# Optimization experiments

Measured on AMD Instinct MI355X. Metric: run time of the kernel, lower is better.

## Reference

```python
import jax, jax.numpy as jnp
import numpy as np

DIM = 512
HEADS = 8
HEAD_DIM = DIM // HEADS


def setup_inputs() -> dict:
    key = jax.random.key(0)
    ks = jax.random.split(key, 8)
    B, T, C, H, W = 2, 8, DIM, 16, 16
    s = lambda fan: 1.0 / np.sqrt(fan)
    return {
        "features_seq": jax.random.normal(ks[0], (B, T, C, H, W), jnp.float32),
        # weights stored as [in, out] (math identical to torch Linear y = x @ W.T)
        "qkv_w": jax.random.normal(ks[1], (C, 3 * C), jnp.float32) * s(C),
        "qkv_b": jnp.zeros((3 * C,), jnp.float32),
        "proj_w": jax.random.normal(ks[2], (C, C), jnp.float32) * s(C),
        "proj_b": jnp.zeros((C,), jnp.float32),
        "ln1_g": jnp.ones((C,), jnp.float32),
        "ln1_b": jnp.zeros((C,), jnp.float32),
        "w1": jax.random.normal(ks[3], (C, 4 * C), jnp.float32) * s(C),
        "b1": jnp.zeros((4 * C,), jnp.float32),
        "w2": jax.random.normal(ks[4], (4 * C, C), jnp.float32) * s(4 * C),
        "b2": jnp.zeros((C,), jnp.float32),
        "ln2_g": jnp.ones((C,), jnp.float32),
        "ln2_b": jnp.zeros((C,), jnp.float32),
    }


def _layernorm(x, g, b, eps=1e-5):
    mu = jnp.mean(x, axis=-1, keepdims=True)
    var = jnp.var(x, axis=-1, keepdims=True)
    return (x - mu) * jax.lax.rsqrt(var + eps) * g + b


def _mhsa(x, qkv_w, qkv_b, proj_w, proj_b):
    B, N, C = x.shape
    qkv = (x @ qkv_w + qkv_b).reshape(B, N, 3, HEADS, HEAD_DIM)
    qkv = jnp.transpose(qkv, (2, 0, 3, 1, 4))  # [3, B, h, N, d]
    q, k, v = qkv[0], qkv[1], qkv[2]
    scale = HEAD_DIM ** -0.5
    attn = jnp.einsum("bhqd,bhkd->bhqk", q, k) * scale
    attn = jax.nn.softmax(attn, axis=-1)
    o = jnp.einsum("bhqk,bhkd->bhqd", attn, v)
    o = jnp.transpose(o, (0, 2, 1, 3)).reshape(B, N, C)
    return o @ proj_w + proj_b


def reference(features_seq, qkv_w, qkv_b, proj_w, proj_b, ln1_g, ln1_b,
              w1, b1, w2, b2, ln2_g, ln2_b):
    B, T, C, H, W = features_seq.shape
    L = H * W
    # [B,T,C,H,W] -> [B, T*L, C]
    x = features_seq.reshape(B, T, C, L).transpose(0, 1, 3, 2).reshape(B, T * L, C)
    x = x + _mhsa(_layernorm(x, ln1_g, ln1_b), qkv_w, qkv_b, proj_w, proj_b)
    h = _layernorm(x, ln2_g, ln2_b)
    h = jax.nn.gelu(h @ w1 + b1, approximate=False) @ w2 + b2
    x = x + h
    # back to [B, T, C, H, W]
    out = x.reshape(B, T, L, C).transpose(0, 1, 3, 2).reshape(B, T, C, H, W)
    return out
```

## Files before the change

kernel.cpp:

```cpp
#include <hip/hip_runtime.h>
#include <stdint.h>
#include <math.h>

typedef __attribute__((ext_vector_type(8))) short short8;
typedef __attribute__((ext_vector_type(4))) float f32x4;
typedef __attribute__((ext_vector_type(4))) ushort ushort4v;

__device__ __forceinline__ ushort f2bf(float f) {
    union { float f; uint32_t i; } v; v.f = f;
    uint32_t r = v.i + 0x7FFFu + ((v.i >> 16) & 1u);
    return (ushort)(r >> 16);
}
__device__ __forceinline__ float bf2f(ushort u) {
    union { uint32_t i; float f; } v; v.i = ((uint32_t)u) << 16; return v.f;
}

__device__ __forceinline__ void gload_lds16(const ushort* gp, ushort* lp) {
    __builtin_amdgcn_global_load_lds(
        (const __attribute__((address_space(1))) void*)gp,
        (__attribute__((address_space(3))) void*)lp, 16, 0, 0);
}

__global__ __launch_bounds__(512) void prep_kernel(const float* __restrict__ in,
        const float* __restrict__ g, const float* __restrict__ bta,
        float* __restrict__ x, ushort* __restrict__ xln) {
    int token = blockIdx.x;
    int c = threadIdx.x;
    int b = token >> 11;
    int n = token & 2047;
    int t = n >> 8;
    int l = n & 255;
    size_t iidx = (((size_t)((b * 8 + t) * 512 + c)) << 8) + l;
    float v = in[iidx];
    x[(size_t)token * 512 + c] = v;

    float s = v, s2 = v * v;
    #pragma unroll
    for (int off = 32; off > 0; off >>= 1) {
        s  += __shfl_down(s, off, 64);
        s2 += __shfl_down(s2, off, 64);
    }
    __shared__ float ps[8], ps2[8];
    int wave = threadIdx.x >> 6, lane = threadIdx.x & 63;
    if (lane == 0) { ps[wave] = s; ps2[wave] = s2; }
    __syncthreads();
    float mu = 0.f, m2 = 0.f;
    #pragma unroll
    for (int i = 0; i < 8; i++) { mu += ps[i]; m2 += ps2[i]; }
    mu *= (1.0f / 512.0f); m2 *= (1.0f / 512.0f);
    float rs = rsqrtf(m2 - mu * mu + 1e-5f);
    float y = (v - mu) * rs * g[c] + bta[c];
    xln[(size_t)token * 512 + c] = f2bf(y);
}

__global__ __launch_bounds__(512) void ln2_kernel(const float* __restrict__ xin,
        const float* __restrict__ g, const float* __restrict__ bta,
        ushort* __restrict__ out) {
    int token = blockIdx.x;
    int c = threadIdx.x;
    float v = xin[(size_t)token * 512 + c];
    float s = v, s2 = v * v;
    #pragma unroll
    for (int off = 32; off > 0; off >>= 1) {
        s  += __shfl_down(s, off, 64);
        s2 += __shfl_down(s2, off, 64);
    }
    __shared__ float ps[8], ps2[8];
    int wave = threadIdx.x >> 6, lane = threadIdx.x & 63;
    if (lane == 0) { ps[wave] = s; ps2[wave] = s2; }
    __syncthreads();
    float mu = 0.f, m2 = 0.f;
    #pragma unroll
    for (int i = 0; i < 8; i++) { mu += ps[i]; m2 += ps2[i]; }
    mu *= (1.0f / 512.0f); m2 *= (1.0f / 512.0f);
    float rs = rsqrtf(m2 - mu * mu + 1e-5f);
    float y = (v - mu) * rs * g[c] + bta[c];
    out[(size_t)token * 512 + c] = f2bf(y);
}

__global__ __launch_bounds__(256) void wtrans_kernel(
        const float* __restrict__ wa, ushort* __restrict__ ta,
        const float* __restrict__ wb, ushort* __restrict__ tb,
        const float* __restrict__ wc, ushort* __restrict__ tc,
        const float* __restrict__ wd, ushort* __restrict__ td) {
    __shared__ float tile[32][33];
    int bid = blockIdx.x;
    const float* W; ushort* T; int K, N, tn, tk;
    if (bid < 768)       { W = wa; T = ta; K = 512;  N = 1536; tn = bid % 48; tk = bid / 48; }
    else if (bid < 1024) { bid -= 768;  W = wb; T = tb; K = 512;  N = 512;  tn = bid % 16; tk = bid / 16; }
    else if (bid < 2048) { bid -= 1024; W = wc; T = tc; K = 512;  N = 2048; tn = bid % 64; tk = bid / 64; }
    else                 { bid -= 2048; W = wd; T = td; K = 2048; N = 512;  tn = bid % 16; tk = bid / 16; }
    int n0 = tn * 32, k0 = tk * 32;
    int tx = threadIdx.x & 31, ty = threadIdx.x >> 5;
    #pragma unroll
    for (int i = 0; i < 4; i++)
        tile[ty + i * 8][tx] = W[(size_t)(k0 + ty + i * 8) * N + n0 + tx];
    __syncthreads();
    #pragma unroll
    for (int i = 0; i < 4; i++) {
        int nn = ty + i * 8;
        T[(size_t)(n0 + nn) * K + k0 + tx] = f2bf(tile[tx][nn]);
    }
}

#define EPI_BF16   0
#define EPI_F32RES 1
#define EPI_GELU   2

template<int EPI>
__global__ __launch_bounds__(256) void gemm_kernel(
        const ushort* __restrict__ A, const ushort* __restrict__ Bt,
        const float* __restrict__ bias, const float* __restrict__ resid,
        float* __restrict__ outF, ushort* __restrict__ outB,
        int M, int N, int K) {
    __shared__ __align__(16) ushort As[2][64 * 64];
    __shared__ __align__(16) ushort Bs[2][128 * 64];
    int tid = threadIdx.x;
    int wave = tid >> 6, lane = tid & 63;
    int l16 = lane & 15, quad = lane >> 4;
    int wc = wave;
    int m0 = blockIdx.y * 64, n0 = blockIdx.x * 128;

    auto stage = [&](int bufi, int k0) {
        ushort* Ab = &As[bufi][0];
        ushort* Bb = &Bs[bufi][0];
        #pragma unroll
        for (int c = 0; c < 2; c++) {
            int e = c * 256 + tid;
            int row = e >> 3, ch = e & 7;
            int sc = ch ^ (row & 7);
            gload_lds16(A + (size_t)(m0 + row) * K + k0 + sc * 8,
                        Ab + (size_t)(c * 256 + wave * 64) * 8);
        }
        #pragma unroll
        for (int c = 0; c < 4; c++) {
            int e = c * 256 + tid;
            int row = e >> 3, ch = e & 7;
            int sc = ch ^ (row & 7);
            gload_lds16(Bt + (size_t)(n0 + row) * K + k0 + sc * 8,
                        Bb + (size_t)(c * 256 + wave * 64) * 8);
        }
    };

    f32x4 acc[4][2] = {};
    stage(0, 0);
    asm volatile("s_waitcnt vmcnt(0)" ::: "memory");
    __builtin_amdgcn_s_barrier();
    __builtin_amdgcn_sched_barrier(0);
    int nt = K >> 6;
    for (int t = 0; t < nt; ++t) {
        int cur = t & 1;
        if (t + 1 < nt) stage(cur ^ 1, (t + 1) << 6);
        const ushort* Ac = &As[cur][0];
        const ushort* Bc = &Bs[cur][0];
        #pragma unroll
        for (int kk = 0; kk < 2; kk++) {
            short8 af[4], bf[2];
            int slot = ((kk * 4 + quad) ^ (l16 & 7)) * 8;
            #pragma unroll
            for (int i = 0; i < 4; i++)
                af[i] = *(const short8*)&Ac[(i * 16 + l16) * 64 + slot];
            #pragma unroll
            for (int j = 0; j < 2; j++)
                bf[j] = *(const short8*)&Bc[(wc * 32 + j * 16 + l16) * 64 + slot];
            #pragma unroll
            for (int i = 0; i < 4; i++)
                #pragma unroll
                for (int j = 0; j < 2; j++)
                    acc[i][j] = __builtin_amdgcn_mfma_f32_16x16x32_bf16(af[i], bf[j], acc[i][j], 0, 0, 0);
        }
        if (t + 1 < nt) {
            asm volatile("s_waitcnt vmcnt(0)" ::: "memory");
            __builtin_amdgcn_s_barrier();
            __builtin_amdgcn_sched_barrier(0);
        }
    }
    #pragma unroll
    for (int i = 0; i < 4; i++) {
        int row_base = m0 + i * 16 + quad * 4;
        #pragma unroll
        for (int j = 0; j < 2; j++) {
            int col = n0 + wc * 32 + j * 16 + l16;
            float bvf = bias[col];
            #pragma unroll
            for (int r = 0; r < 4; r++) {
                int row = row_base + r;
                float v = acc[i][j][r] + bvf;
                if constexpr (EPI == EPI_F32RES) {
                    outF[(size_t)row * N + col] = v + resid[(size_t)row * N + col];
                } else if constexpr (EPI == EPI_GELU) {
                    float gg = 0.5f * v * (1.0f + erff(v * 0.70710678118654752f));
                    outB[(size_t)row * N + col] = f2bf(gg);
                } else {
                    outB[(size_t)row * N + col] = f2bf(v);
                }
            }
        }
    }
}

__global__ __launch_bounds__(512, 6) void flash_kernel(const ushort* __restrict__ qkv,
        ushort* __restrict__ o) {
    __shared__ __align__(16) char smem[47232];
    auto Ks  = (ushort (*)[64][72])smem;
    auto Vt  = (ushort (*)[4640])(smem + 18432);
    auto Pt  = (ushort (*)[16][40])(smem + 36992);
    auto cbuf = (float (*)[18][64])smem;

    int tid = threadIdx.x;
    int wave = tid >> 6, lane = tid & 63;
    int kh = wave >> 2;
    int wq = wave & 3;
    int l16 = lane & 15, quad = lane >> 4;
    int bidx = blockIdx.x;
    int qt = bidx & 31;
    int h = (bidx >> 5) & 7;
    int b = bidx >> 8;
    int q0 = qt * 64;
    const size_t base = (size_t)b * 2048 * 1536;

    int htid = tid & 255;
    int srow = htid >> 2;
    int sg   = htid & 3;
    int sdb  = sg * 16;
    const ushort* kgbase = qkv + base + 512  + h * 64 + sdb;
    const ushort* vgbase = qkv + base + 1024 + h * 64 + sdb;
    int vldsoff = sdb * 72 + sg * 8 + srow;

    short8 aq[2];
    {
        int qrow = q0 + wq * 16 + l16;
        const ushort* qp = qkv + base + (size_t)qrow * 1536 + h * 64;
        aq[0] = *(const short8*)(qp + quad * 8);
        aq[1] = *(const short8*)(qp + 32 + quad * 8);
    }
    f32x4 accO[4] = {};
    float mrow = -INFINITY, lrow = 0.f;

    {
        int kb = kh * 1024;
        const ushort* kp = kgbase + (size_t)(kb + srow) * 1536;
        short8 k0 = *(const short8*)kp;
        short8 k1 = *(const short8*)(kp + 8);
        const ushort* vp = vgbase + (size_t)(kb + srow) * 1536;
        short8 v0 = *(const short8*)vp;
        short8 v1 = *(const short8*)(vp + 8);
        *(short8*)&Ks[kh][srow][sdb]     = k0;
        *(short8*)&Ks[kh][srow][sdb + 8] = k1;
        #pragma unroll
        for (int i = 0; i < 8; i++) Vt[kh][vldsoff + i * 72] = (ushort)v0[i];
        #pragma unroll
        for (int i = 0; i < 8; i++) Vt[kh][vldsoff + (8 + i) * 72] = (ushort)v1[i];
    }
    __syncthreads();

    for (int it = 0; it < 16; ++it) {
        short8 nk0, nk1, nv0, nv1;
        bool pre = (it < 15);
        if (pre) {
            int kb = kh * 1024 + (it + 1) * 64;
            const ushort* kp = kgbase + (size_t)(kb + srow) * 1536;
            nk0 = *(const short8*)kp;
            nk1 = *(const short8*)(kp + 8);
            const ushort* vp = vgbase + (size_t)(kb + srow) * 1536;
            nv0 = *(const short8*)vp;
            nv1 = *(const short8*)(vp + 8);
        }
        f32x4 sacc[4] = {};
        __builtin_amdgcn_s_setprio(1);
        #pragma unroll
        for (int c = 0; c < 2; c++) {
            #pragma unroll
            for (int s = 0; s < 4; s++) {
                short8 kf = *(short8*)&Ks[kh][s * 16 + l16][c * 32 + quad * 8];
                sacc[s] = __builtin_amdgcn_mfma_f32_16x16x32_bf16(kf, aq[c], sacc[s], 0, 0, 0);
            }
        }
        __builtin_amdgcn_s_setprio(0);
        float tm = sacc[0][0];
        #pragma unroll
        for (int s = 0; s < 4; s++)
            #pragma unroll
            for (int r = 0; r < 4; r++) tm = fmaxf(tm, sacc[s][r]);
        tm = fmaxf(tm, __shfl_xor(tm, 16, 64));
        tm = fmaxf(tm, __shfl_xor(tm, 32, 64));
        float mn = fmaxf(mrow, tm * 0.125f);
        float al = __expf(mrow - mn);
        float rsum = 0.f;
        ushort4v w4[4];
        #pragma unroll
        for (int s = 0; s < 4; s++)
            #pragma unroll
            for (int r = 0; r < 4; r++) {
                float pv = __expf(sacc[s][r] * 0.125f - mn);
                rsum += pv;
                w4[s][r] = f2bf(pv);
            }
        rsum += __shfl_xor(rsum, 16, 64);
        rsum += __shfl_xor(rsum, 32, 64);
        lrow = lrow * al + rsum;
        mrow = mn;
        #pragma unroll
        for (int s = 0; s < 4; s++)
            #pragma unroll
            for (int r = 0; r < 4; r++) accO[s][r] *= al;
        *(ushort4v*)&Pt[wave][l16][quad * 4]      = w4[0];
        *(ushort4v*)&Pt[wave][l16][16 + quad * 4] = w4[1];
        {
            short8 ap = *(short8*)&Pt[wave][l16][quad * 8];
            __builtin_amdgcn_s_setprio(1);
            #pragma unroll
            for (int s = 0; s < 4; s++) {
                short8 vf = *(short8*)&Vt[kh][(s * 16 + l16) * 72 + s * 8 + quad * 8];
                accO[s] = __builtin_amdgcn_mfma_f32_16x16x32_bf16(vf, ap, accO[s], 0, 0, 0);
            }
            __builtin_amdgcn_s_setprio(0);
        }
        *(ushort4v*)&Pt[wave][l16][quad * 4]      = w4[2];
        *(ushort4v*)&Pt[wave][l16][16 + quad * 4] = w4[3];
        {
            short8 ap = *(short8*)&Pt[wave][l16][quad * 8];
            __builtin_amdgcn_s_setprio(1);
            #pragma unroll
            for (int s = 0; s < 4; s++) {
                short8 vf = *(short8*)&Vt[kh][(s * 16 + l16) * 72 + s * 8 + 32 + quad * 8];
                accO[s] = __builtin_amdgcn_mfma_f32_16x16x32_bf16(vf, ap, accO[s], 0, 0, 0);
            }
            __builtin_amdgcn_s_setprio(0);
        }
        __syncthreads();
        if (pre) {
            *(short8*)&Ks[kh][srow][sdb]     = nk0;
            *(short8*)&Ks[kh][srow][sdb + 8] = nk1;
            #pragma unroll
            for (int i = 0; i < 8; i++) Vt[kh][vldsoff + i * 72] = (ushort)nv0[i];
            #pragma unroll
            for (int i = 0; i < 8; i++) Vt[kh][vldsoff + (8 + i) * 72] = (ushort)nv1[i];
        }
        __syncthreads();
    }
    if (kh == 1) {
        cbuf[wq][0][lane] = mrow;
        cbuf[wq][1][lane] = lrow;
        #pragma unroll
        for (int s = 0; s < 4; s++)
            #pragma unroll
            for (int r = 0; r < 4; r++)
                cbuf[wq][2 + s * 4 + r][lane] = accO[s][r];
    }
    __syncthreads();
    if (kh == 0) {
        float m1 = cbuf[wq][0][lane];
        float l1 = cbuf[wq][1][lane];
        float mn = fmaxf(mrow, m1);
        float a0 = __expf(mrow - mn);
        float a1 = __expf(m1 - mn);
        float rl = 1.0f / (lrow * a0 + l1 * a1);
        int qrow = q0 + wq * 16 + l16;
        #pragma unroll
        for (int s = 0; s < 4; s++) {
            ushort4v ov4;
            #pragma unroll
            for (int r = 0; r < 4; r++) {
                float ov = (accO[s][r] * a0 + cbuf[wq][2 + s * 4 + r][lane] * a1) * rl;
                ov4[r] = f2bf(ov);
            }
            *(ushort4v*)&o[((size_t)(b * 2048 + qrow)) * 512 + h * 64 + s * 16 + quad * 4] = ov4;
        }
    }
}

__global__ __launch_bounds__(256) void tout_kernel(const float* __restrict__ x3,
        float* __restrict__ out) {
    __shared__ float tile[32][33];
    int bt = blockIdx.z;
    int l0 = blockIdx.y * 32;
    int c0 = blockIdx.x * 32;
    int tx = threadIdx.x, ty = threadIdx.y;
    #pragma unroll
    for (int i = 0; i < 4; i++) {
        int l = ty + i * 8;
        tile[l][tx] = x3[((size_t)bt * 256 + l0 + l) * 512 + c0 + tx];
    }
    __syncthreads();
    #pragma unroll
    for (int i = 0; i < 4; i++) {
        int cc = ty + i * 8;
        out[((size_t)bt * 512 + c0 + cc) * 256 + l0 + tx] = tile[tx][cc];
    }
}

extern "C" void kernel_launch(void* const* d_in, const int* in_sizes, int n_in,
                              void* d_out, int out_size, void* d_ws, size_t ws_size,
                              hipStream_t stream) {
    const float* in_feat = (const float*)d_in[0];
    const float* qkv_w  = (const float*)d_in[1];
    const float* qkv_b  = (const float*)d_in[2];
    const float* proj_w = (const float*)d_in[3];
    const float* proj_b = (const float*)d_in[4];
    const float* ln1_g  = (const float*)d_in[5];
    const float* ln1_b  = (const float*)d_in[6];
    const float* w1     = (const float*)d_in[7];
    const float* b1     = (const float*)d_in[8];
    const float* w2     = (const float*)d_in[9];
    const float* b2     = (const float*)d_in[10];
    const float* ln2_g  = (const float*)d_in[11];
    const float* ln2_b  = (const float*)d_in[12];

    char* ws = (char*)d_ws;
    float*  x    = (float*) (ws);
    float*  x2   = (float*) (ws + 8388608);
    ushort* xln  = (ushort*)(ws + 16777216);
    ushort* h2   = (ushort*)(ws + 20971520);
    ushort* ao   = (ushort*)(ws + 25165824);
    ushort* qkv  = (ushort*)(ws + 29360128);
    ushort* gbuf = (ushort*)(ws + 41943040);

    char* scr = (char*)d_out;
    ushort* qkvT = (ushort*)(scr);
    ushort* projT = (ushort*)(scr + 1572864);
    ushort* w1T  = (ushort*)(scr + 2097152);
    ushort* w2T  = (ushort*)(scr + 4194304);

    wtrans_kernel<<<3072, 256, 0, stream>>>(qkv_w, qkvT, proj_w, projT,
                                            w1, w1T, w2, w2T);
    prep_kernel<<<4096, 512, 0, stream>>>(in_feat, ln1_g, ln1_b, x, xln);
    gemm_kernel<EPI_BF16><<<dim3(12, 64), 256, 0, stream>>>(
        xln, qkvT, qkv_b, nullptr, nullptr, qkv, 4096, 1536, 512);
    flash_kernel<<<512, 512, 0, stream>>>(qkv, ao);
    gemm_kernel<EPI_F32RES><<<dim3(4, 64), 256, 0, stream>>>(
        ao, projT, proj_b, x, x2, nullptr, 4096, 512, 512);
    ln2_kernel<<<4096, 512, 0, stream>>>(x2, ln2_g, ln2_b, h2);
    gemm_kernel<EPI_GELU><<<dim3(16, 64), 256, 0, stream>>>(
        h2, w1T, b1, nullptr, nullptr, gbuf, 4096, 2048, 512);
    gemm_kernel<EPI_F32RES><<<dim3(4, 64), 256, 0, stream>>>(
        gbuf, w2T, b2, x2, x, nullptr, 4096, 512, 2048);
    tout_kernel<<<dim3(16, 8, 16), dim3(32, 8), 0, stream>>>(x, (float*)d_out);
}
```

Before: 242.6 us.

## Switch GEMM to 128x128 tiles with register-staged padded LDS loads

The GEMM kernel moves from 64x128 tiles with direct global-to-LDS async loads and XOR swizzle to 128x128 tiles. Each wave now computes a 64x64 sub-tile. K steps are 32 wide, and operands are prefetched into registers and then written into padded LDS rows (stride 36). The aim is more MFMA reuse per loaded byte and fewer tiles. In exchange it halves the grid, which leaves only 128 blocks for the N=512 GEMMs, and it drops the async LDS loads. The flash kernel's occupancy hint is also removed.

```diff
diff --git a/kernel.cpp b/kernel.cpp
--- a/kernel.cpp
+++ b/kernel.cpp
@@ -13,12 +13,6 @@
 }
 __device__ __forceinline__ float bf2f(ushort u) {
     union { uint32_t i; float f; } v; v.i = ((uint32_t)u) << 16; return v.f;
-}
-
-__device__ __forceinline__ void gload_lds16(const ushort* gp, ushort* lp) {
-    __builtin_amdgcn_global_load_lds(
-        (const __attribute__((address_space(1))) void*)gp,
-        (__attribute__((address_space(3))) void*)lp, 16, 0, 0);
 }
 
 __global__ __launch_bounds__(512) void prep_kernel(const float* __restrict__ in,
@@ -108,79 +102,74 @@
 #define EPI_GELU   2
 
 template<int EPI>
-__global__ __launch_bounds__(256) void gemm_kernel(
+__global__ __launch_bounds__(256, 3) void gemm_kernel(
         const ushort* __restrict__ A, const ushort* __restrict__ Bt,
         const float* __restrict__ bias, const float* __restrict__ resid,
         float* __restrict__ outF, ushort* __restrict__ outB,
         int M, int N, int K) {
-    __shared__ __align__(16) ushort As[2][64 * 64];
-    __shared__ __align__(16) ushort Bs[2][128 * 64];
+    __shared__ __align__(16) ushort As[2][128 * 36];
+    __shared__ __align__(16) ushort Bs[2][128 * 36];
     int tid = threadIdx.x;
     int wave = tid >> 6, lane = tid & 63;
     int l16 = lane & 15, quad = lane >> 4;
-    int wc = wave;
-    int m0 = blockIdx.y * 64, n0 = blockIdx.x * 128;
-
-    auto stage = [&](int bufi, int k0) {
-        ushort* Ab = &As[bufi][0];
-        ushort* Bb = &Bs[bufi][0];
-        #pragma unroll
-        for (int c = 0; c < 2; c++) {
-            int e = c * 256 + tid;
-            int row = e >> 3, ch = e & 7;
-            int sc = ch ^ (row & 7);
-            gload_lds16(A + (size_t)(m0 + row) * K + k0 + sc * 8,
-                        Ab + (size_t)(c * 256 + wave * 64) * 8);
-        }
-        #pragma unroll
-        for (int c = 0; c < 4; c++) {
-            int e = c * 256 + tid;
-            int row = e >> 3, ch = e & 7;
-            int sc = ch ^ (row & 7);
-            gload_lds16(Bt + (size_t)(n0 + row) * K + k0 + sc * 8,
-                        Bb + (size_t)(c * 256 + wave * 64) * 8);
-        }
-    };
-
-    f32x4 acc[4][2] = {};
-    stage(0, 0);
-    asm volatile("s_waitcnt vmcnt(0)" ::: "memory");
-    __builtin_amdgcn_s_barrier();
-    __builtin_amdgcn_sched_barrier(0);
-    int nt = K >> 6;
+    int wr = wave >> 1, wc = wave & 1;
+    int m0 = blockIdx.y * 128, n0 = blockIdx.x * 128;
+
+    int r0 = tid >> 2;
+    int ch = tid & 3;
+    const ushort* Ag0 = A  + (size_t)(m0 + r0) * K + ch * 8;
+    const ushort* Ag1 = A  + (size_t)(m0 + 64 + r0) * K + ch * 8;
+    const ushort* Bg0 = Bt + (size_t)(n0 + r0) * K + ch * 8;
+    const ushort* Bg1 = Bt + (size_t)(n0 + 64 + r0) * K + ch * 8;
+    int w0 = r0 * 36 + ch * 8;
+    int w1 = (64 + r0) * 36 + ch * 8;
+
+    f32x4 acc[4][4] = {};
+    short8 pa0, pa1, pb0, pb1;
+
+    pa0 = *(const short8*)(Ag0); pa1 = *(const short8*)(Ag1);
+    pb0 = *(const short8*)(Bg0); pb1 = *(const short8*)(Bg1);
+    *(short8*)&As[0][w0] = pa0;  *(short8*)&As[0][w1] = pa1;
+    *(short8*)&Bs[0][w0] = pb0;  *(short8*)&Bs[0][w1] = pb1;
+    __syncthreads();
+
+    int nt = K >> 5;
     for (int t = 0; t < nt; ++t) {
         int cur = t & 1;
-        if (t + 1 < nt) stage(cur ^ 1, (t + 1) << 6);
+        if (t + 1 < nt) {
+            int kt = (t + 1) << 5;
+            pa0 = *(const short8*)(Ag0 + kt); pa1 = *(const short8*)(Ag1 + kt);
+            pb0 = *(const short8*)(Bg0 + kt); pb1 = *(const short8*)(Bg1 + kt);
+        }
         const ushort* Ac = &As[cur][0];
         const ushort* Bc = &Bs[cur][0];
-        #pragma unroll
-        for (int kk = 0; kk < 2; kk++) {
-            short8 af[4], bf[2];
-            int slot = ((kk * 4 + quad) ^ (l16 & 7)) * 8;
-            #pragma unroll
-            for (int i = 0; i < 4; i++)
-                af[i] = *(const short8*)&Ac[(i * 16 + l16) * 64 + slot];
-            #pragma unroll
-            for (int j = 0; j < 2; j++)
-                bf[j] = *(const short8*)&Bc[(wc * 32 + j * 16 + l16) * 64 + slot];
-            #pragma unroll
-            for (int i = 0; i < 4; i++)
-                #pragma unroll
-                for (int j = 0; j < 2; j++)
-                    acc[i][j] = __builtin_amdgcn_mfma_f32_16x16x32_bf16(af[i], bf[j], acc[i][j], 0, 0, 0);
-        }
+        short8 af[4], bf[4];
+        #pragma unroll
+        for (int i = 0; i < 4; i++)
+            af[i] = *(const short8*)&Ac[(wr * 64 + i * 16 + l16) * 36 + quad * 8];
+        #pragma unroll
+        for (int j = 0; j < 4; j++)
+            bf[j] = *(const short8*)&Bc[(wc * 64 + j * 16 + l16) * 36 + quad * 8];
+        #pragma unroll
+        for (int i = 0; i < 4; i++)
+            #pragma unroll
+            for (int j = 0; j < 4; j++)
+                acc[i][j] = __builtin_amdgcn_mfma_f32_16x16x32_bf16(af[i], bf[j], acc[i][j], 0, 0, 0);
+        __builtin_amdgcn_s_barrier();
+        __builtin_amdgcn_sched_barrier(0);
         if (t + 1 < nt) {
-            asm volatile("s_waitcnt vmcnt(0)" ::: "memory");
-            __builtin_amdgcn_s_barrier();
-            __builtin_amdgcn_sched_barrier(0);
+            int nxt = cur ^ 1;
+            *(short8*)&As[nxt][w0] = pa0;  *(short8*)&As[nxt][w1] = pa1;
+            *(short8*)&Bs[nxt][w0] = pb0;  *(short8*)&Bs[nxt][w1] = pb1;
+            __syncthreads();
         }
     }
     #pragma unroll
     for (int i = 0; i < 4; i++) {
-        int row_base = m0 + i * 16 + quad * 4;
-        #pragma unroll
-        for (int j = 0; j < 2; j++) {
-            int col = n0 + wc * 32 + j * 16 + l16;
+        int row_base = m0 + wr * 64 + i * 16 + quad * 4;
+        #pragma unroll
+        for (int j = 0; j < 4; j++) {
+            int col = n0 + wc * 64 + j * 16 + l16;
             float bvf = bias[col];
             #pragma unroll
             for (int r = 0; r < 4; r++) {
@@ -199,7 +188,7 @@
     }
 }
 
-__global__ __launch_bounds__(512, 6) void flash_kernel(const ushort* __restrict__ qkv,
+__global__ __launch_bounds__(512) void flash_kernel(const ushort* __restrict__ qkv,
         ushort* __restrict__ o) {
     __shared__ __align__(16) char smem[47232];
     auto Ks  = (ushort (*)[64][72])smem;
@@ -425,15 +414,15 @@
     wtrans_kernel<<<3072, 256, 0, stream>>>(qkv_w, qkvT, proj_w, projT,
                                             w1, w1T, w2, w2T);
     prep_kernel<<<4096, 512, 0, stream>>>(in_feat, ln1_g, ln1_b, x, xln);
-    gemm_kernel<EPI_BF16><<<dim3(12, 64), 256, 0, stream>>>(
+    gemm_kernel<EPI_BF16><<<dim3(12, 32), 256, 0, stream>>>(
         xln, qkvT, qkv_b, nullptr, nullptr, qkv, 4096, 1536, 512);
     flash_kernel<<<512, 512, 0, stream>>>(qkv, ao);
-    gemm_kernel<EPI_F32RES><<<dim3(4, 64), 256, 0, stream>>>(
+    gemm_kernel<EPI_F32RES><<<dim3(4, 32), 256, 0, stream>>>(
         ao, projT, proj_b, x, x2, nullptr, 4096, 512, 512);
     ln2_kernel<<<4096, 512, 0, stream>>>(x2, ln2_g, ln2_b, h2);
-    gemm_kernel<EPI_GELU><<<dim3(16, 64), 256, 0, stream>>>(
+    gemm_kernel<EPI_GELU><<<dim3(16, 32), 256, 0, stream>>>(
         h2, w1T, b1, nullptr, nullptr, gbuf, 4096, 2048, 512);
-    gemm_kernel<EPI_F32RES><<<dim3(4, 64), 256, 0, stream>>>(
+    gemm_kernel<EPI_F32RES><<<dim3(4, 32), 256, 0, stream>>>(
         gbuf, w2T, b2, x2, x, nullptr, 4096, 512, 2048);
     tout_kernel<<<dim3(16, 8, 16), dim3(32, 8), 0, stream>>>(x, (float*)d_out);
 }
```

Measured after the change: 334.9 us. 38.0% more time.

## Add 128-row GEMM tiles and drop LDS double buffering

Applied to the files above, without the earlier changes.

Templates the GEMM on block-row size, using 128x128 tiles with a 2x2 wave layout for the QKV and FC1 GEMMs to raise operand reuse per LDS load. Replaces the double-buffered prefetch pipeline with a single-buffer load/sync/compute loop, reducing LDS use but removing overlap of global loads with MFMA work. Also removes the min-blocks occupancy hint from the attention kernel.

```diff
diff --git a/kernel.cpp b/kernel.cpp
--- a/kernel.cpp
+++ b/kernel.cpp
@@ -107,30 +107,32 @@
 #define EPI_F32RES 1
 #define EPI_GELU   2
 
-template<int EPI>
+template<int EPI, int BM>
 __global__ __launch_bounds__(256) void gemm_kernel(
         const ushort* __restrict__ A, const ushort* __restrict__ Bt,
         const float* __restrict__ bias, const float* __restrict__ resid,
         float* __restrict__ outF, ushort* __restrict__ outB,
         int M, int N, int K) {
-    __shared__ __align__(16) ushort As[2][64 * 64];
-    __shared__ __align__(16) ushort Bs[2][128 * 64];
+    __shared__ __align__(16) ushort As[BM * 64];
+    __shared__ __align__(16) ushort Bs[128 * 64];
     int tid = threadIdx.x;
     int wave = tid >> 6, lane = tid & 63;
     int l16 = lane & 15, quad = lane >> 4;
-    int wc = wave;
-    int m0 = blockIdx.y * 64, n0 = blockIdx.x * 128;
-
-    auto stage = [&](int bufi, int k0) {
-        ushort* Ab = &As[bufi][0];
-        ushort* Bb = &Bs[bufi][0];
-        #pragma unroll
-        for (int c = 0; c < 2; c++) {
+    constexpr int NJ = (BM == 128) ? 4 : 2;
+    constexpr int WCW = (BM == 128) ? 64 : 32;
+    int wr = (BM == 128) ? (wave >> 1) : 0;
+    int wc = (BM == 128) ? (wave & 1) : wave;
+    int m0 = blockIdx.y * BM, n0 = blockIdx.x * 128;
+
+    f32x4 acc[4][NJ] = {};
+    for (int k0 = 0; k0 < K; k0 += 64) {
+        #pragma unroll
+        for (int c = 0; c < BM / 32; c++) {
             int e = c * 256 + tid;
             int row = e >> 3, ch = e & 7;
             int sc = ch ^ (row & 7);
             gload_lds16(A + (size_t)(m0 + row) * K + k0 + sc * 8,
-                        Ab + (size_t)(c * 256 + wave * 64) * 8);
+                        As + (size_t)(c * 256 + wave * 64) * 8);
         }
         #pragma unroll
         for (int c = 0; c < 4; c++) {
@@ -138,49 +140,36 @@
             int row = e >> 3, ch = e & 7;
             int sc = ch ^ (row & 7);
             gload_lds16(Bt + (size_t)(n0 + row) * K + k0 + sc * 8,
-                        Bb + (size_t)(c * 256 + wave * 64) * 8);
-        }
-    };
-
-    f32x4 acc[4][2] = {};
-    stage(0, 0);
-    asm volatile("s_waitcnt vmcnt(0)" ::: "memory");
-    __builtin_amdgcn_s_barrier();
-    __builtin_amdgcn_sched_barrier(0);
-    int nt = K >> 6;
-    for (int t = 0; t < nt; ++t) {
-        int cur = t & 1;
-        if (t + 1 < nt) stage(cur ^ 1, (t + 1) << 6);
-        const ushort* Ac = &As[cur][0];
-        const ushort* Bc = &Bs[cur][0];
+                        Bs + (size_t)(c * 256 + wave * 64) * 8);
+        }
+        __syncthreads();
         #pragma unroll
         for (int kk = 0; kk < 2; kk++) {
-            short8 af[4], bf[2];
-            int slot = ((kk * 4 + quad) ^ (l16 & 7)) * 8;
-            #pragma unroll
-            for (int i = 0; i < 4; i++)
-                af[i] = *(const short8*)&Ac[(i * 16 + l16) * 64 + slot];
-            #pragma unroll
-            for (int j = 0; j < 2; j++)
-                bf[j] = *(const short8*)&Bc[(wc * 32 + j * 16 + l16) * 64 + slot];
+            short8 af[4], bf[NJ];
+            #pragma unroll
+            for (int i = 0; i < 4; i++) {
+                int row = wr * 64 + i * 16 + l16;
+                af[i] = *(const short8*)&As[row * 64 + ((kk * 4 + quad) ^ (row & 7)) * 8];
+            }
+            #pragma unroll
+            for (int j = 0; j < NJ; j++) {
+                int row = wc * WCW + j * 16 + l16;
+                bf[j] = *(const short8*)&Bs[row * 64 + ((kk * 4 + quad) ^ (row & 7)) * 8];
+            }
             #pragma unroll
             for (int i = 0; i < 4; i++)
                 #pragma unroll
-                for (int j = 0; j < 2; j++)
+                for (int j = 0; j < NJ; j++)
                     acc[i][j] = __builtin_amdgcn_mfma_f32_16x16x32_bf16(af[i], bf[j], acc[i][j], 0, 0, 0);
         }
-        if (t + 1 < nt) {
-            asm volatile("s_waitcnt vmcnt(0)" ::: "memory");
-            __builtin_amdgcn_s_barrier();
-            __builtin_amdgcn_sched_barrier(0);
-        }
+        __syncthreads();
     }
     #pragma unroll
     for (int i = 0; i < 4; i++) {
-        int row_base = m0 + i * 16 + quad * 4;
-        #pragma unroll
-        for (int j = 0; j < 2; j++) {
-            int col = n0 + wc * 32 + j * 16 + l16;
+        int row_base = m0 + wr * 64 + i * 16 + quad * 4;
+        #pragma unroll
+        for (int j = 0; j < NJ; j++) {
+            int col = n0 + wc * WCW + j * 16 + l16;
             float bvf = bias[col];
             #pragma unroll
             for (int r = 0; r < 4; r++) {
@@ -199,7 +188,7 @@
     }
 }
 
-__global__ __launch_bounds__(512, 6) void flash_kernel(const ushort* __restrict__ qkv,
+__global__ __launch_bounds__(512) void flash_kernel(const ushort* __restrict__ qkv,
         ushort* __restrict__ o) {
     __shared__ __align__(16) char smem[47232];
     auto Ks  = (ushort (*)[64][72])smem;
@@ -425,15 +414,15 @@
     wtrans_kernel<<<3072, 256, 0, stream>>>(qkv_w, qkvT, proj_w, projT,
                                             w1, w1T, w2, w2T);
     prep_kernel<<<4096, 512, 0, stream>>>(in_feat, ln1_g, ln1_b, x, xln);
-    gemm_kernel<EPI_BF16><<<dim3(12, 64), 256, 0, stream>>>(
+    gemm_kernel<EPI_BF16, 128><<<dim3(12, 32), 256, 0, stream>>>(
         xln, qkvT, qkv_b, nullptr, nullptr, qkv, 4096, 1536, 512);
     flash_kernel<<<512, 512, 0, stream>>>(qkv, ao);
-    gemm_kernel<EPI_F32RES><<<dim3(4, 64), 256, 0, stream>>>(
+    gemm_kernel<EPI_F32RES, 64><<<dim3(4, 64), 256, 0, stream>>>(
         ao, projT, proj_b, x, x2, nullptr, 4096, 512, 512);
     ln2_kernel<<<4096, 512, 0, stream>>>(x2, ln2_g, ln2_b, h2);
-    gemm_kernel<EPI_GELU><<<dim3(16, 64), 256, 0, stream>>>(
+    gemm_kernel<EPI_GELU, 128><<<dim3(16, 32), 256, 0, stream>>>(
         h2, w1T, b1, nullptr, nullptr, gbuf, 4096, 2048, 512);
-    gemm_kernel<EPI_F32RES><<<dim3(4, 64), 256, 0, stream>>>(
+    gemm_kernel<EPI_F32RES, 64><<<dim3(4, 64), 256, 0, stream>>>(
         gbuf, w2T, b2, x2, x, nullptr, 4096, 512, 2048);
     tout_kernel<<<dim3(16, 8, 16), dim3(32, 8), 0, stream>>>(x, (float*)d_out);
 }
```

After: 241.7 us. No clear change (-0.4%).

## Split-K the final MLP GEMM and fold partial sums into output transpose

Applied to the files above, without the earlier changes.

The last GEMM (K=2048) is launched with a z-dimension of 2. Each half writes unbiased fp32 partials to separate workspace buffers, and the output transpose kernel adds the two partials, the residual and b2. This doubles the block count for a GEMM that otherwise has only 256 tiles. The shared GEMM kernel also loses its double-buffered LDS staging and the XOR swizzle, going to a simple load/sync/compute loop. That risks LDS bank conflicts and lost load/compute overlap in every GEMM. The flash kernel's occupancy hint in launch_bounds is dropped as well.

```diff
diff --git a/kernel.cpp b/kernel.cpp
--- a/kernel.cpp
+++ b/kernel.cpp
@@ -103,91 +103,77 @@
     }
 }
 
-#define EPI_BF16   0
-#define EPI_F32RES 1
-#define EPI_GELU   2
+#define EPI_BF16    0
+#define EPI_F32RES  1
+#define EPI_GELU    2
+#define EPI_F32PART 3
 
 template<int EPI>
 __global__ __launch_bounds__(256) void gemm_kernel(
         const ushort* __restrict__ A, const ushort* __restrict__ Bt,
         const float* __restrict__ bias, const float* __restrict__ resid,
-        float* __restrict__ outF, ushort* __restrict__ outB,
-        int M, int N, int K) {
-    __shared__ __align__(16) ushort As[2][64 * 64];
-    __shared__ __align__(16) ushort Bs[2][128 * 64];
+        float* __restrict__ outF, float* __restrict__ outF2,
+        ushort* __restrict__ outB, int M, int N, int K) {
+    __shared__ __align__(16) ushort As[64 * 64];
+    __shared__ __align__(16) ushort Bs[128 * 64];
     int tid = threadIdx.x;
     int wave = tid >> 6, lane = tid & 63;
     int l16 = lane & 15, quad = lane >> 4;
     int wc = wave;
     int m0 = blockIdx.y * 64, n0 = blockIdx.x * 128;
-
-    auto stage = [&](int bufi, int k0) {
-        ushort* Ab = &As[bufi][0];
-        ushort* Bb = &Bs[bufi][0];
+    int Ksp = K / gridDim.z;
+    int kbeg = blockIdx.z * Ksp, kend = kbeg + Ksp;
+
+    f32x4 acc[4][2] = {};
+    for (int k0 = kbeg; k0 < kend; k0 += 64) {
         #pragma unroll
         for (int c = 0; c < 2; c++) {
-            int e = c * 256 + tid;
-            int row = e >> 3, ch = e & 7;
-            int sc = ch ^ (row & 7);
-            gload_lds16(A + (size_t)(m0 + row) * K + k0 + sc * 8,
-                        Ab + (size_t)(c * 256 + wave * 64) * 8);
+            int slot = c * 256 + tid;
+            int row = slot >> 3, ch = slot & 7;
+            gload_lds16(A + (size_t)(m0 + row) * K + k0 + ch * 8,
+                        As + (size_t)(c * 256 + wave * 64) * 8);
         }
         #pragma unroll
         for (int c = 0; c < 4; c++) {
-            int e = c * 256 + tid;
-            int row = e >> 3, ch = e & 7;
-            int sc = ch ^ (row & 7);
-            gload_lds16(Bt + (size_t)(n0 + row) * K + k0 + sc * 8,
-                        Bb + (size_t)(c * 256 + wave * 64) * 8);
-        }
-    };
-
-    f32x4 acc[4][2] = {};
-    stage(0, 0);
-    asm volatile("s_waitcnt vmcnt(0)" ::: "memory");
-    __builtin_amdgcn_s_barrier();
-    __builtin_amdgcn_sched_barrier(0);
-    int nt = K >> 6;
-    for (int t = 0; t < nt; ++t) {
-        int cur = t & 1;
-        if (t + 1 < nt) stage(cur ^ 1, (t + 1) << 6);
-        const ushort* Ac = &As[cur][0];
-        const ushort* Bc = &Bs[cur][0];
+            int slot = c * 256 + tid;
+            int row = slot >> 3, ch = slot & 7;
+            gload_lds16(Bt + (size_t)(n0 + row) * K + k0 + ch * 8,
+                        Bs + (size_t)(c * 256 + wave * 64) * 8);
+        }
+        __syncthreads();
         #pragma unroll
         for (int kk = 0; kk < 2; kk++) {
             short8 af[4], bf[2];
-            int slot = ((kk * 4 + quad) ^ (l16 & 7)) * 8;
             #pragma unroll
             for (int i = 0; i < 4; i++)
-                af[i] = *(const short8*)&Ac[(i * 16 + l16) * 64 + slot];
+                af[i] = *(const short8*)&As[(i * 16 + l16) * 64 + kk * 32 + quad * 8];
             #pragma unroll
             for (int j = 0; j < 2; j++)
-                bf[j] = *(const short8*)&Bc[(wc * 32 + j * 16 + l16) * 64 + slot];
+                bf[j] = *(const short8*)&Bs[(wc * 32 + j * 16 + l16) * 64 + kk * 32 + quad * 8];
             #pragma unroll
             for (int i = 0; i < 4; i++)
                 #pragma unroll
                 for (int j = 0; j < 2; j++)
                     acc[i][j] = __builtin_amdgcn_mfma_f32_16x16x32_bf16(af[i], bf[j], acc[i][j], 0, 0, 0);
         }
-        if (t + 1 < nt) {
-            asm volatile("s_waitcnt vmcnt(0)" ::: "memory");
-            __builtin_amdgcn_s_barrier();
-            __builtin_amdgcn_sched_barrier(0);
-        }
-    }
+        __syncthreads();
+    }
+    float* oP = (EPI == EPI_F32PART && blockIdx.z == 1) ? outF2 : outF;
     #pragma unroll
     for (int i = 0; i < 4; i++) {
         int row_base = m0 + i * 16 + quad * 4;
         #pragma unroll
         for (int j = 0; j < 2; j++) {
             int col = n0 + wc * 32 + j * 16 + l16;
-            float bvf = bias[col];
+            float bvf = (EPI == EPI_F32PART) ? 0.f : bias[col];
             #pragma unroll
             for (int r = 0; r < 4; r++) {
                 int row = row_base + r;
                 float v = acc[i][j][r] + bvf;
                 if constexpr (EPI == EPI_F32RES) {
                     outF[(size_t)row * N + col] = v + resid[(size_t)row * N + col];
+                } else if constexpr (EPI == EPI_F32PART) {
+                    oP[(size_t)row * N + col] = v;
                 } else if constexpr (EPI == EPI_GELU) {
                     float gg = 0.5f * v * (1.0f + erff(v * 0.70710678118654752f));
                     outB[(size_t)row * N + col] = f2bf(gg);
@@ -199,7 +185,7 @@
     }
 }
 
-__global__ __launch_bounds__(512, 6) void flash_kernel(const ushort* __restrict__ qkv,
+__global__ __launch_bounds__(512) void flash_kernel(const ushort* __restrict__ qkv,
         ushort* __restrict__ o) {
     __shared__ __align__(16) char smem[47232];
     auto Ks  = (ushort (*)[64][72])smem;
@@ -370,17 +356,20 @@
     }
 }
 
-__global__ __launch_bounds__(256) void tout_kernel(const float* __restrict__ x3,
-        float* __restrict__ out) {
+__global__ __launch_bounds__(256) void tout_kernel(const float* __restrict__ x2,
+        const float* __restrict__ pA, const float* __restrict__ pB,
+        const float* __restrict__ b2, float* __restrict__ out) {
     __shared__ float tile[32][33];
     int bt = blockIdx.z;
     int l0 = blockIdx.y * 32;
     int c0 = blockIdx.x * 32;
     int tx = threadIdx.x, ty = threadIdx.y;
+    float bv = b2[c0 + tx];
     #pragma unroll
     for (int i = 0; i < 4; i++) {
         int l = ty + i * 8;
-        tile[l][tx] = x3[((size_t)bt * 256 + l0 + l) * 512 + c0 + tx];
+        size_t idx = ((size_t)bt * 256 + l0 + l) * 512 + c0 + tx;
+        tile[l][tx] = x2[idx] + pA[idx] + pB[idx] + bv;
     }
     __syncthreads();
     #pragma unroll
@@ -416,6 +405,9 @@
     ushort* qkv  = (ushort*)(ws + 29360128);
     ushort* gbuf = (ushort*)(ws + 41943040);
 
+    float* pA = (float*)(ws);
+    float* pB = (float*)(ws + 16777216);
+
     char* scr = (char*)d_out;
     ushort* qkvT = (ushort*)(scr);
     ushort* projT = (ushort*)(scr + 1572864);
@@ -426,14 +418,15 @@
                                             w1, w1T, w2, w2T);
     prep_kernel<<<4096, 512, 0, stream>>>(in_feat, ln1_g, ln1_b, x, xln);
     gemm_kernel<EPI_BF16><<<dim3(12, 64), 256, 0, stream>>>(
-        xln, qkvT, qkv_b, nullptr, nullptr, qkv, 4096, 1536, 512);
+        xln, qkvT, qkv_b, nullptr, nullptr, nullptr, qkv, 4096, 1536, 512);
     flash_kernel<<<512, 512, 0, stream>>>(qkv, ao);
     gemm_kernel<EPI_F32RES><<<dim3(4, 64), 256, 0, stream>>>(
-        ao, projT, proj_b, x, x2, nullptr, 4096, 512, 512);
+        ao, projT, proj_b, x, x2, nullptr, nullptr, 4096, 512, 512);
     ln2_kernel<<<4096, 512, 0, stream>>>(x2, ln2_g, ln2_b, h2);
     gemm_kernel<EPI_GELU><<<dim3(16, 64), 256, 0, stream>>>(
-        h2, w1T, b1, nullptr, nullptr, gbuf, 4096, 2048, 512);
-    gemm_kernel<EPI_F32RES><<<dim3(4, 64), 256, 0, stream>>>(
-        gbuf, w2T, b2, x2, x, nullptr, 4096, 512, 2048);
-    tout_kernel<<<dim3(16, 8, 16), dim3(32, 8), 0, stream>>>(x, (float*)d_out);
-}
+        h2, w1T, b1, nullptr, nullptr, nullptr, gbuf, 4096, 2048, 512);
+    gemm_kernel<EPI_F32PART><<<dim3(4, 64, 2), 256, 0, stream>>>(
+        gbuf, w2T, nullptr, nullptr, pA, pB, nullptr, 4096, 512, 2048);
+    tout_kernel<<<dim3(16, 8, 16), dim3(32, 8), 0, stream>>>(
+        x2, pA, pB, b2, (float*)d_out);
+}
```

New measurement: 230.3 us. 5.1% less time.
